# Performance work log

Hardware: AMD Instinct MI355X
Metric: run time of the kernel (lower is better)

## Reference

```python
import jax, jax.numpy as jnp
import numpy as np

D_MODEL = 1024
D_KV = 64
N_HEADS = 16
KV_HEADS = 4
G = N_HEADS // KV_HEADS
NUM_BUCKETS = 32
MAX_DISTANCE = 128


def _relative_position_bucket(relative_position, bidirectional=True,
                              num_buckets=NUM_BUCKETS, max_distance=MAX_DISTANCE):
    # Faithful port of T5Attention._relative_position_bucket
    relative_buckets = jnp.zeros_like(relative_position)
    if bidirectional:
        num_buckets //= 2
        relative_buckets = (relative_position > 0).astype(jnp.int32) * num_buckets
        relative_position = jnp.abs(relative_position)
    else:
        relative_position = -jnp.minimum(relative_position, 0)
    max_exact = num_buckets // 2
    is_small = relative_position < max_exact
    rel_if_large = max_exact + (
        jnp.log(relative_position.astype(jnp.float32) / max_exact)
        / np.log(max_distance / max_exact) * (num_buckets - max_exact)
    ).astype(jnp.int32)
    rel_if_large = jnp.minimum(rel_if_large, num_buckets - 1)
    return relative_buckets + jnp.where(is_small, relative_position, rel_if_large)


def setup_inputs() -> dict:
    key = jax.random.key(0)
    ks = jax.random.split(key, 6)
    B, S = 2, 2048
    inner = N_HEADS * D_KV
    sc = 1.0 / np.sqrt(D_MODEL)
    return {
        "hidden_states": jax.random.normal(ks[0], (B, S, D_MODEL), dtype=jnp.float32),
        "Wq": jax.random.normal(ks[1], (D_MODEL, inner), dtype=jnp.float32) * sc,
        "Wk": jax.random.normal(ks[2], (D_MODEL, inner), dtype=jnp.float32) * sc,
        "Wv": jax.random.normal(ks[3], (D_MODEL, inner), dtype=jnp.float32) * sc,
        "Wo": jax.random.normal(ks[4], (inner, D_MODEL), dtype=jnp.float32) * sc,
        "rel_bias": jax.random.normal(ks[5], (NUM_BUCKETS, N_HEADS), dtype=jnp.float32) * 0.1,
    }


def reference(hidden_states, Wq, Wk, Wv, Wo, rel_bias):
    B, S, _ = hidden_states.shape

    def split_heads(x):  # [B,S,inner] -> [B,H,S,Dk]
        return x.reshape(B, S, N_HEADS, D_KV).transpose(0, 2, 1, 3)

    q = split_heads(hidden_states @ Wq)
    k = split_heads(hidden_states @ Wk)
    v = split_heads(hidden_states @ Wv)

    # head index = g * KV_HEADS + h (einops 'b (g h) ...' with h=kv_heads)
    gq = q.reshape(B, G, KV_HEADS, S, D_KV)
    gk = k.reshape(B, G, KV_HEADS, S, D_KV).mean(axis=1)  # [B,Hkv,S,Dk]
    # einsum sums over g (as in torch.einsum 'bghnd,bhsd->bhns'); no 1/sqrt(d) in T5
    scores = jnp.einsum('bghnd,bhsd->bhns', gq, gk)  # [B,Hkv,S,S]

    # T5 relative position bias (bidirectional, encoder)
    ctx = jnp.arange(S)[:, None]
    mem = jnp.arange(S)[None, :]
    buckets = _relative_position_bucket(mem - ctx, bidirectional=True)
    bias = rel_bias[buckets]                # [S,S,H]
    bias = bias.transpose(2, 0, 1)[None]    # [1,H,S,S]
    gbias = bias.reshape(1, G, KV_HEADS, S, S).mean(axis=1)  # [1,Hkv,S,S]

    scores = scores + gbias
    attn = jax.nn.softmax(scores.astype(jnp.float32), axis=-1).astype(scores.dtype)

    # repeat grouped attn weights back to full heads: 'b h n s -> b (g h) n s'
    attn_full = jnp.tile(attn, (1, G, 1, 1))  # [B,H,S,S]
    ctx_out = jnp.einsum('bhns,bhsd->bhnd', attn_full, v)  # [B,H,S,Dk]
    ctx_out = ctx_out.transpose(0, 2, 1, 3).reshape(B, S, N_HEADS * D_KV)
    return ctx_out @ Wo  # [B,S,D_MODEL]
```

## Files before the change

### kernel.cpp

```cpp
#include <hip/hip_runtime.h>
#include <math.h>


typedef __bf16 bf16_t;
typedef bf16_t bf16x8 __attribute__((ext_vector_type(8)));
typedef bf16_t bf16x4 __attribute__((ext_vector_type(4)));
typedef float f32x4 __attribute__((ext_vector_type(4)));

#define MFMA16(a, b, c) __builtin_amdgcn_mfma_f32_16x16x32_bf16(a, b, c, 0, 0, 0)

typedef __attribute__((address_space(1))) void gvoid;
typedef __attribute__((address_space(3))) void svoid;
__device__ __forceinline__ void gld16(const void* g, void* l) {
    __builtin_amdgcn_global_load_lds((gvoid*)g, (svoid*)l, 16, 0, 0);
}

__global__ __launch_bounds__(256) void prep_all(const float* __restrict__ hs,
                                                const float* __restrict__ Wq,
                                                const float* __restrict__ Wk,
                                                const float* __restrict__ Wv,
                                                const float* __restrict__ Wo,
                                                const float* __restrict__ rel_bias,
                                                bf16_t* __restrict__ hs_hi,
                                                bf16_t* __restrict__ hs_lo,
                                                bf16_t* __restrict__ Thi,
                                                bf16_t* __restrict__ Tlo,
                                                bf16_t* __restrict__ WvT,
                                                bf16_t* __restrict__ WoT,
                                                float* __restrict__ btab) {
    __shared__ float sm[2048];
    const int r = blockIdx.x, t = threadIdx.x;
    if (r < 4096) {
        size_t idx = ((size_t)r * 256 + t) * 4;
        float4 v = *(const float4*)(hs + idx);
        bf16x4 h, l;
        h[0] = (bf16_t)v.x; l[0] = (bf16_t)(v.x - (float)h[0]);
        h[1] = (bf16_t)v.y; l[1] = (bf16_t)(v.y - (float)h[1]);
        h[2] = (bf16_t)v.z; l[2] = (bf16_t)(v.z - (float)h[2]);
        h[3] = (bf16_t)v.w; l[3] = (bf16_t)(v.w - (float)h[3]);
        *(bf16x4*)(hs_hi + idx) = h;
        *(bf16x4*)(hs_lo + idx) = l;
    } else if (r < 5120) {
        int k = r - 4096;
        float* rq = sm;
        float* rk = sm + 1024;
#pragma unroll
        for (int j = 0; j < 4; ++j) {
            rq[t + j * 256] = Wq[(size_t)k * 1024 + t + j * 256];
            rk[t + j * 256] = Wk[(size_t)k * 1024 + t + j * 256];
        }
        __syncthreads();
        int h = t >> 6, j2 = t & 63;
        float sq = 0.f, sk = 0.f;
#pragma unroll
        for (int g = 0; g < 4; ++g) {
            sq += rq[(g * 4 + h) * 64 + j2];
            sk += rk[(g * 4 + h) * 64 + j2];
        }
        sk *= 0.25f;
        bf16_t qh = (bf16_t)sq;
        Thi[(size_t)t * 1024 + k] = qh;
        Tlo[(size_t)t * 1024 + k] = (bf16_t)(sq - (float)qh);
        bf16_t kh = (bf16_t)sk;
        Thi[(size_t)(256 + t) * 1024 + k] = kh;
        Tlo[(size_t)(256 + t) * 1024 + k] = (bf16_t)(sk - (float)kh);
    } else if (r < 7168) {
        const float* src = (r < 6144) ? Wv : Wo;
        bf16_t* dst = (r < 6144) ? WvT : WoT;
        int rr = (r < 6144) ? r - 5120 : r - 6144;
        int bx = (rr & 31) * 32, by = (rr >> 5) * 32;
        int tx = t & 31, ty = t >> 5;
        float(*tile)[33] = (float(*)[33])sm;
#pragma unroll
        for (int i = 0; i < 32; i += 8)
            tile[ty + i][tx] = src[(size_t)(by + ty + i) * 1024 + bx + tx];
        __syncthreads();
#pragma unroll
        for (int i = 0; i < 32; i += 8)
            dst[(size_t)(bx + ty + i) * 1024 + by + tx] = (bf16_t)tile[tx][ty + i];
    } else {
        int idx = (r - 7168) * 256 + t;
        if (idx >= 4095) return;
        int delta = idx - 2047;
        int bucket = (delta > 0) ? 16 : 0;
        int arp = delta < 0 ? -delta : delta;
        int rb;
        if (arp < 8) {
            rb = arp;
        } else {
            float tt = (logf((float)arp * 0.125f) / 2.772588722239781f) * 8.0f;
            int ri = 8 + (int)tt;
            rb = ri < 15 ? ri : 15;
        }
        bucket += rb;
#pragma unroll
        for (int h = 0; h < 4; ++h) {
            float s = 0.25f * (rel_bias[bucket * 16 + h] + rel_bias[bucket * 16 + h + 4] +
                               rel_bias[bucket * 16 + h + 8] + rel_bias[bucket * 16 + h + 12]);
            btab[h * 4608 + idx] = s;
        }
    }
}

__global__ __launch_bounds__(256, 1) void proj_qkv(const bf16_t* __restrict__ Ah,
                                                   const bf16_t* __restrict__ Al,
                                                   const bf16_t* __restrict__ Bh,
                                                   const bf16_t* __restrict__ Bl,
                                                   const bf16_t* __restrict__ WvT,
                                                   bf16_t* __restrict__ Qhi,
                                                   bf16_t* __restrict__ Qlo,
                                                   bf16_t* __restrict__ Kbh,
                                                   bf16_t* __restrict__ Kbl,
                                                   bf16_t* __restrict__ Vb) {
    __shared__ bf16_t pool[24576];
    const int K = 1024, nk = 32;
    const int t = threadIdx.x;
    const int w = t >> 6, lane = t & 63;
    const int lr = lane & 15, q = lane >> 4;
    const int bx = blockIdx.x;
    const bool qk = bx < 8;
    const int m0 = blockIdx.y * 128;
    const int n0 = qk ? bx * 64 : (bx - 8) * 128;
    const int mw = (w & 1) * 64;
    f32x4 acc[4][4] = {};

    const int rA = t & 127, cA0 = t >> 7, cA1 = 2 + (t >> 7);
    const size_t oA0 = (size_t)(m0 + rA) * K + cA0 * 8;
    const size_t oA1 = (size_t)(m0 + rA) * K + cA1 * 8;
    const int rBq = t & 63, cBq = t >> 6;
    const size_t oBq = (size_t)(n0 + rBq) * K + cBq * 8;
    const size_t oBv0 = (size_t)(n0 + rA) * K + cA0 * 8;
    const size_t oBv1 = (size_t)(n0 + rA) * K + cA1 * 8;

    auto stage = [&](int bf, int k0) {
        gld16(Ah + oA0 + k0, &pool[bf * 4096 + t * 8]);
        gld16(Ah + oA1 + k0, &pool[bf * 4096 + (256 + t) * 8]);
        if (qk) {
            gld16(Al + oA0 + k0, &pool[8192 + bf * 4096 + t * 8]);
            gld16(Al + oA1 + k0, &pool[8192 + bf * 4096 + (256 + t) * 8]);
            gld16(Bh + oBq + k0, &pool[16384 + bf * 2048 + t * 8]);
            gld16(Bl + oBq + k0, &pool[20480 + bf * 2048 + t * 8]);
        } else {
            gld16(WvT + oBv0 + k0, &pool[8192 + bf * 4096 + t * 8]);
            gld16(WvT + oBv1 + k0, &pool[8192 + bf * 4096 + (256 + t) * 8]);
        }
    };

    stage(0, 0);
    __syncthreads();
    for (int it = 0; it < nk; ++it) {
        const int cur = it & 1;
        if (it + 1 < nk) stage(cur ^ 1, (it + 1) * 32);
        if (qk) {
            const int nw = (w >> 1) * 32;
            bf16x8 ah[4], al[4], bh[2], bl[2];
#pragma unroll
            for (int i = 0; i < 4; ++i) {
                int sa = (q * 128 + mw + i * 16 + lr) * 8;
                ah[i] = *(const bf16x8*)&pool[cur * 4096 + sa];
                al[i] = *(const bf16x8*)&pool[8192 + cur * 4096 + sa];
            }
#pragma unroll
            for (int j = 0; j < 2; ++j) {
                int sb = (q * 64 + nw + j * 16 + lr) * 8;
                bh[j] = *(const bf16x8*)&pool[16384 + cur * 2048 + sb];
                bl[j] = *(const bf16x8*)&pool[20480 + cur * 2048 + sb];
            }
#pragma unroll
            for (int i = 0; i < 4; ++i)
#pragma unroll
                for (int j = 0; j < 2; ++j) {
                    acc[i][j] = MFMA16(ah[i], bh[j], acc[i][j]);
                    acc[i][j] = MFMA16(ah[i], bl[j], acc[i][j]);
                    acc[i][j] = MFMA16(al[i], bh[j], acc[i][j]);
                }
        } else {
            const int nw = (w >> 1) * 64;
            bf16x8 af[4], bfv[4];
#pragma unroll
            for (int i = 0; i < 4; ++i)
                af[i] = *(const bf16x8*)&pool[cur * 4096 + (q * 128 + mw + i * 16 + lr) * 8];
#pragma unroll
            for (int j = 0; j < 4; ++j)
                bfv[j] =
                    *(const bf16x8*)&pool[8192 + cur * 4096 + (q * 128 + nw + j * 16 + lr) * 8];
#pragma unroll
            for (int i = 0; i < 4; ++i)
#pragma unroll
                for (int j = 0; j < 4; ++j) acc[i][j] = MFMA16(af[i], bfv[j], acc[i][j]);
        }
        __syncthreads();
    }

    const int nj = qk ? 2 : 4;
    const int nwq = qk ? (w >> 1) * 32 : (w >> 1) * 64;
#pragma unroll
    for (int i = 0; i < 4; ++i) {
        int row = m0 + mw + i * 16 + q * 4;
#pragma unroll 4
        for (int j = 0; j < nj; ++j) {
            int col = n0 + nwq + j * 16 + lr;
#pragma unroll
            for (int reg = 0; reg < 4; ++reg) {
                float x = acc[i][j][reg];
                int token = row + reg;
                if (qk) {
                    bf16_t hi = (bf16_t)x;
                    bf16_t lo = (bf16_t)(x - (float)hi);
                    if (col < 256) {
                        size_t o = (size_t)token * 256 + col;
                        Qhi[o] = hi;
                        Qlo[o] = lo;
                    } else {
                        int hc = col - 256;
                        int h = hc >> 6, d = hc & 63;
                        int b = token >> 11, s = token & 2047;
                        int it2 = s >> 6, sl = s & 63;
                        size_t o = ((size_t)((b * 4 + h) * 32 + it2)) * 4096 +
                                   (size_t)((d >> 3) * 64 + sl) * 8 + (d & 7);
                        Kbh[o] = hi;
                        Kbl[o] = lo;
                    }
                } else {
                    int vg = col;
                    int h = (vg >> 6) & 3, g = vg >> 8, d = vg & 63;
                    int b = token >> 11, s = token & 2047;
                    int it2 = s >> 6, sc = (s >> 3) & 7, si = s & 7;
                    size_t o = ((size_t)((b * 4 + h) * 32 + it2)) * 16384 +
                               (size_t)(sc * 256 + g * 64 + d) * 8 + si;
                    Vb[o] = (bf16_t)x;
                }
            }
        }
    }
}

__global__ __launch_bounds__(256, 1) void gemm_out(const bf16_t* __restrict__ A,
                                                   const bf16_t* __restrict__ BT,
                                                   float* __restrict__ C,
                                                   int M, int N, int K) {
    __shared__ bf16_t pool[12288];
    const int t = threadIdx.x;
    const int w = t >> 6, lane = t & 63;
    const int lr = lane & 15, q = lane >> 4;
    const int m0 = blockIdx.y * 128, n0 = blockIdx.x * 64;
    const int mw = (w & 1) * 64, nw = (w >> 1) * 32;
    f32x4 acc[4][2] = {};
    const int nk = K >> 5;

    const int rA = t & 127, cA0 = t >> 7, cA1 = 2 + (t >> 7);
    const bf16_t* gA0 = A + (size_t)(m0 + rA) * K + cA0 * 8;
    const bf16_t* gA1 = A + (size_t)(m0 + rA) * K + cA1 * 8;
    const bf16_t* gB = BT + (size_t)(n0 + (t & 63)) * K + (t >> 6) * 8;

    auto stage = [&](int bf, int k0) {
        gld16(gA0 + k0, &pool[bf * 4096 + t * 8]);
        gld16(gA1 + k0, &pool[bf * 4096 + (256 + t) * 8]);
        gld16(gB + k0, &pool[8192 + bf * 2048 + t * 8]);
    };

    stage(0, 0);
    __syncthreads();
    for (int it = 0; it < nk; ++it) {
        const int cur = it & 1;
        if (it + 1 < nk) stage(cur ^ 1, (it + 1) * 32);
        bf16x8 af[4], bfv[2];
#pragma unroll
        for (int i = 0; i < 4; ++i)
            af[i] = *(const bf16x8*)&pool[cur * 4096 + (q * 128 + mw + i * 16 + lr) * 8];
#pragma unroll
        for (int j = 0; j < 2; ++j)
            bfv[j] = *(const bf16x8*)&pool[8192 + cur * 2048 + (q * 64 + nw + j * 16 + lr) * 8];
#pragma unroll
        for (int i = 0; i < 4; ++i)
#pragma unroll
            for (int j = 0; j < 2; ++j) acc[i][j] = MFMA16(af[i], bfv[j], acc[i][j]);
        __syncthreads();
    }

#pragma unroll
    for (int i = 0; i < 4; ++i) {
        int row = m0 + mw + i * 16 + q * 4;
#pragma unroll
        for (int j = 0; j < 2; ++j) {
            int col = n0 + nw + j * 16 + lr;
#pragma unroll
            for (int reg = 0; reg < 4; ++reg)
                C[(size_t)(row + reg) * N + col] = acc[i][j][reg];
        }
    }
}

__global__ __launch_bounds__(512, 1) void attn_mfma(const bf16_t* __restrict__ Qhi,
                                                    const bf16_t* __restrict__ Qlo,
                                                    const bf16_t* __restrict__ Kbh,
                                                    const bf16_t* __restrict__ Kbl,
                                                    const bf16_t* __restrict__ Vb,
                                                    const float* __restrict__ btab,
                                                    bf16_t* __restrict__ part0,
                                                    bf16_t* __restrict__ part1,
                                                    float* __restrict__ Sml) {
    __shared__ bf16_t Kh[2][4096], Kl[2][4096], Vsm[2][16384], Ps[8192];
    const int t = threadIdx.x, w = t >> 6, lane = t & 63;
    const int lr = lane & 15, q = lane >> 4;
    const int blk = blockIdx.x;
    const int half = blk & 1, qt = (blk >> 1) & 15, h = (blk >> 5) & 3, b = blk >> 7;
    const int n0 = qt * 128;
    const int rowbase = n0 + w * 16;

    const size_t qrow = (size_t)(b * 2048 + rowbase + lr) * 256 + h * 64;
    bf16x8 aqh[2], aql[2];
#pragma unroll
    for (int kb = 0; kb < 2; ++kb) {
        aqh[kb] = *(const bf16x8*)(Qhi + qrow + kb * 32 + q * 8);
        aql[kb] = *(const bf16x8*)(Qlo + qrow + kb * 32 + q * 8);
    }

    const int tilebase = (b * 4 + h) * 32 + half * 16;
    const bf16_t* gK = Kbh + (size_t)tilebase * 4096;
    const bf16_t* gL = Kbl + (size_t)tilebase * 4096;
    const bf16_t* gV = Vb + (size_t)tilebase * 16384;
    const float* btabh = btab + h * 4608 + 2047;

    auto stage = [&](int bf, int it) {
        gld16(gK + (size_t)it * 4096 + t * 8, &Kh[bf][t * 8]);
        gld16(gL + (size_t)it * 4096 + t * 8, &Kl[bf][t * 8]);
        const bf16_t* v0 = gV + (size_t)it * 16384;
#pragma unroll
        for (int j = 0; j < 4; ++j)
            gld16(v0 + (j * 512 + t) * 8, &Vsm[bf][(j * 512 + t) * 8]);
    };

    float m_r[4], l_r[4];
#pragma unroll
    for (int reg = 0; reg < 4; ++reg) { m_r[reg] = -INFINITY; l_r[reg] = 0.f; }
    f32x4 O[16] = {};

    stage(0, 0);
    __syncthreads();
    for (int it = 0; it < 16; ++it) {
        const int cur = it & 1;
        if (it + 1 < 16) stage(cur ^ 1, it + 1);
        const int s0g = half * 1024 + it * 64;

        f32x4 sc[4];
#pragma unroll
        for (int ct = 0; ct < 4; ++ct) {
            f32x4 z = {0.f, 0.f, 0.f, 0.f};
#pragma unroll
            for (int kb = 0; kb < 2; ++kb) {
                int sb = ((kb * 4 + q) * 64 + ct * 16 + lr) * 8;
                bf16x8 bh = *(const bf16x8*)&Kh[cur][sb];
                bf16x8 bl = *(const bf16x8*)&Kl[cur][sb];
                z = MFMA16(aqh[kb], bh, z);
                z = MFMA16(aqh[kb], bl, z);
                z = MFMA16(aql[kb], bh, z);
            }
            sc[ct] = z;
        }
        const int dbase = (s0g + lr) - (rowbase + q * 4);
#pragma unroll
        for (int ct = 0; ct < 4; ++ct)
#pragma unroll
            for (int reg = 0; reg < 4; ++reg)
                sc[ct][reg] += btabh[dbase + ct * 16 - reg];

        float rm[4];
#pragma unroll
        for (int reg = 0; reg < 4; ++reg)
            rm[reg] = fmaxf(fmaxf(sc[0][reg], sc[1][reg]), fmaxf(sc[2][reg], sc[3][reg]));
#pragma unroll
        for (int off = 1; off < 16; off <<= 1)
#pragma unroll
            for (int reg = 0; reg < 4; ++reg)
                rm[reg] = fmaxf(rm[reg], __shfl_xor(rm[reg], off, 64));

        float alpha[4], rs[4];
#pragma unroll
        for (int reg = 0; reg < 4; ++reg) {
            float mo = m_r[reg];
            float mn = fmaxf(mo, rm[reg]);
            alpha[reg] = __expf(mo - mn);
            m_r[reg] = mn;
            rs[reg] = 0.f;
        }
#pragma unroll
        for (int ct = 0; ct < 4; ++ct) {
#pragma unroll
            for (int reg = 0; reg < 4; ++reg) {
                float p = __expf(sc[ct][reg] - m_r[reg]);
                rs[reg] += p;
                int col = ct * 16 + lr;
                Ps[((w * 128 + (col >> 3) * 16) + q * 4 + reg) * 8 + (col & 7)] = (bf16_t)p;
            }
        }
#pragma unroll
        for (int off = 1; off < 16; off <<= 1)
#pragma unroll
            for (int reg = 0; reg < 4; ++reg) rs[reg] += __shfl_xor(rs[reg], off, 64);
#pragma unroll
        for (int reg = 0; reg < 4; ++reg) l_r[reg] = l_r[reg] * alpha[reg] + rs[reg];

        bf16x8 pa[2];
#pragma unroll
        for (int kb = 0; kb < 2; ++kb)
            pa[kb] = *(const bf16x8*)&Ps[(w * 128 + (kb * 4 + q) * 16 + lr) * 8];

#pragma unroll
        for (int nt = 0; nt < 16; ++nt) {
            f32x4 o = O[nt];
#pragma unroll
            for (int reg = 0; reg < 4; ++reg) o[reg] *= alpha[reg];
#pragma unroll
            for (int kb = 0; kb < 2; ++kb) {
                bf16x8 v = *(const bf16x8*)&Vsm[cur][((kb * 4 + q) * 256 + nt * 16 + lr) * 8];
                o = MFMA16(pa[kb], v, o);
            }
            O[nt] = o;
        }
        __syncthreads();
    }

    bf16_t* P = half ? part1 : part0;
    float inv[4];
#pragma unroll
    for (int reg = 0; reg < 4; ++reg) inv[reg] = 1.f / l_r[reg];
    const size_t tokbase = (size_t)(b * 2048 + rowbase + q * 4);
#pragma unroll
    for (int nt = 0; nt < 16; ++nt) {
        int v = nt * 16 + lr;
        int vg = ((v >> 6) * 4 + h) * 64 + (v & 63);
#pragma unroll
        for (int reg = 0; reg < 4; ++reg)
            P[(tokbase + reg) * 1024 + vg] = (bf16_t)(O[nt][reg] * inv[reg]);
    }
    if (lr == 0) {
#pragma unroll
        for (int reg = 0; reg < 4; ++reg)
            Sml[half * 16384 + (tokbase + reg) * 4 + h] = m_r[reg] + logf(l_r[reg]);
    }
}

__global__ __launch_bounds__(256) void combine_halves(bf16_t* __restrict__ p0,
                                                      const bf16_t* __restrict__ p1,
                                                      const float* __restrict__ Sml) {
    size_t flat = ((size_t)blockIdx.x * 256 + threadIdx.x) * 8;
    int tok = (int)(flat >> 10), c = (int)(flat & 1023), h = (c >> 6) & 3;
    float s0 = Sml[tok * 4 + h], s1 = Sml[16384 + tok * 4 + h];
    float M = fmaxf(s0, s1);
    float e0 = __expf(s0 - M), e1 = __expf(s1 - M);
    float r = 1.f / (e0 + e1);
    float w0 = e0 * r, w1 = e1 * r;
    bf16x8 a = *(bf16x8*)(p0 + flat);
    bf16x8 bb = *(const bf16x8*)(p1 + flat);
    bf16x8 o;
#pragma unroll
    for (int i = 0; i < 8; ++i) o[i] = (bf16_t)(w0 * (float)a[i] + w1 * (float)bb[i]);
    *(bf16x8*)(p0 + flat) = o;
}

extern "C" void kernel_launch(void* const* d_in, const int* in_sizes, int n_in,
                              void* d_out, int out_size, void* d_ws, size_t ws_size,
                              hipStream_t stream) {
    const float* hs = (const float*)d_in[0];
    const float* Wq = (const float*)d_in[1];
    const float* Wk = (const float*)d_in[2];
    const float* Wv = (const float*)d_in[3];
    const float* Wo = (const float*)d_in[4];
    const float* rb = (const float*)d_in[5];
    float* out = (float*)d_out;

    const size_t MB = 1 << 20;
    const size_t KB = 1 << 10;
    char* ws = (char*)d_ws;
    bf16_t* hs_hi = (bf16_t*)(ws);
    bf16_t* hs_lo = (bf16_t*)(ws + 8 * MB);
    bf16_t* WqkThi = (bf16_t*)(ws + 16 * MB);
    bf16_t* WqkTlo = (bf16_t*)(ws + 17 * MB);
    bf16_t* WvT = (bf16_t*)(ws + 18 * MB);
    bf16_t* WoT = (bf16_t*)(ws + 20 * MB);
    float* btab = (float*)(ws + 22 * MB);
    float* Sml = (float*)(ws + 22 * MB + 128 * KB);
    bf16_t* Qhi = (bf16_t*)(ws + 22 * MB + 256 * KB);
    bf16_t* Qlo = Qhi + (size_t)4096 * 256;
    bf16_t* Kbh = Qlo + (size_t)4096 * 256;
    bf16_t* Kbl = Kbh + (size_t)4096 * 256;
    bf16_t* Vb = Kbl + (size_t)4096 * 256;
    bf16_t* part0 = hs_hi;
    bf16_t* part1 = hs_lo;

    prep_all<<<7184, 256, 0, stream>>>(hs, Wq, Wk, Wv, Wo, rb, hs_hi, hs_lo, WqkThi,
                                       WqkTlo, WvT, WoT, btab);
    proj_qkv<<<dim3(16, 32), 256, 0, stream>>>(hs_hi, hs_lo, WqkThi, WqkTlo, WvT, Qhi,
                                               Qlo, Kbh, Kbl, Vb);
    attn_mfma<<<256, 512, 0, stream>>>(Qhi, Qlo, Kbh, Kbl, Vb, btab, part0, part1, Sml);
    combine_halves<<<2048, 256, 0, stream>>>(part0, part1, Sml);
    gemm_out<<<dim3(16, 32), 256, 0, stream>>>(part0, WoT, out, 4096, 1024, 1024);
}
```

Measured before the change: 241.0 us.

## Retile attention to 64-row query blocks with 32-key tiles and 256 threads

Shrinks the attention kernel's work per block to 64 query rows and 32-key tiles with 256 threads, doubling the grid to 512 blocks, and adjusts the K/V packed layouts accordingly. The QKV projection's V path is narrowed to 64-column tiles, increasing its grid. The aim is better CU occupancy and load balance on a wide GPU, at the cost of more loop iterations, more syncs and softmax rescaling per key element.

```diff
diff --git a/kernel.cpp b/kernel.cpp
--- a/kernel.cpp
+++ b/kernel.cpp
@@ -120,29 +120,25 @@
     const int bx = blockIdx.x;
     const bool qk = bx < 8;
     const int m0 = blockIdx.y * 128;
-    const int n0 = qk ? bx * 64 : (bx - 8) * 128;
-    const int mw = (w & 1) * 64;
-    f32x4 acc[4][4] = {};
+    const int n0 = qk ? bx * 64 : (bx - 8) * 64;
+    const int mw = (w & 1) * 64, nw = (w >> 1) * 32;
+    f32x4 acc[4][2] = {};
 
     const int rA = t & 127, cA0 = t >> 7, cA1 = 2 + (t >> 7);
     const size_t oA0 = (size_t)(m0 + rA) * K + cA0 * 8;
     const size_t oA1 = (size_t)(m0 + rA) * K + cA1 * 8;
-    const int rBq = t & 63, cBq = t >> 6;
-    const size_t oBq = (size_t)(n0 + rBq) * K + cBq * 8;
-    const size_t oBv0 = (size_t)(n0 + rA) * K + cA0 * 8;
-    const size_t oBv1 = (size_t)(n0 + rA) * K + cA1 * 8;
+    const int rB = t & 63, cB = t >> 6;
+    const size_t oB = (size_t)(n0 + rB) * K + cB * 8;
+    const bf16_t* Bhi = qk ? Bh : WvT;
 
     auto stage = [&](int bf, int k0) {
         gld16(Ah + oA0 + k0, &pool[bf * 4096 + t * 8]);
         gld16(Ah + oA1 + k0, &pool[bf * 4096 + (256 + t) * 8]);
+        gld16(Bhi + oB + k0, &pool[16384 + bf * 2048 + t * 8]);
         if (qk) {
             gld16(Al + oA0 + k0, &pool[8192 + bf * 4096 + t * 8]);
             gld16(Al + oA1 + k0, &pool[8192 + bf * 4096 + (256 + t) * 8]);
-            gld16(Bh + oBq + k0, &pool[16384 + bf * 2048 + t * 8]);
-            gld16(Bl + oBq + k0, &pool[20480 + bf * 2048 + t * 8]);
-        } else {
-            gld16(WvT + oBv0 + k0, &pool[8192 + bf * 4096 + t * 8]);
-            gld16(WvT + oBv1 + k0, &pool[8192 + bf * 4096 + (256 + t) * 8]);
+            gld16(Bl + oB + k0, &pool[20480 + bf * 2048 + t * 8]);
         }
     };
 
@@ -152,7 +148,6 @@
         const int cur = it & 1;
         if (it + 1 < nk) stage(cur ^ 1, (it + 1) * 32);
         if (qk) {
-            const int nw = (w >> 1) * 32;
             bf16x8 ah[4], al[4], bh[2], bl[2];
 #pragma unroll
             for (int i = 0; i < 4; ++i) {
@@ -175,31 +170,27 @@
                     acc[i][j] = MFMA16(al[i], bh[j], acc[i][j]);
                 }
         } else {
-            const int nw = (w >> 1) * 64;
-            bf16x8 af[4], bfv[4];
+            bf16x8 af[4], bfv[2];
 #pragma unroll
             for (int i = 0; i < 4; ++i)
                 af[i] = *(const bf16x8*)&pool[cur * 4096 + (q * 128 + mw + i * 16 + lr) * 8];
 #pragma unroll
-            for (int j = 0; j < 4; ++j)
-                bfv[j] =
-                    *(const bf16x8*)&pool[8192 + cur * 4096 + (q * 128 + nw + j * 16 + lr) * 8];
+            for (int j = 0; j < 2; ++j)
+                bfv[j] = *(const bf16x8*)&pool[16384 + cur * 2048 + (q * 64 + nw + j * 16 + lr) * 8];
 #pragma unroll
             for (int i = 0; i < 4; ++i)
 #pragma unroll
-                for (int j = 0; j < 4; ++j) acc[i][j] = MFMA16(af[i], bfv[j], acc[i][j]);
+                for (int j = 0; j < 2; ++j) acc[i][j] = MFMA16(af[i], bfv[j], acc[i][j]);
         }
         __syncthreads();
     }
 
-    const int nj = qk ? 2 : 4;
-    const int nwq = qk ? (w >> 1) * 32 : (w >> 1) * 64;
 #pragma unroll
     for (int i = 0; i < 4; ++i) {
         int row = m0 + mw + i * 16 + q * 4;
-#pragma unroll 4
-        for (int j = 0; j < nj; ++j) {
-            int col = n0 + nwq + j * 16 + lr;
+#pragma unroll
+        for (int j = 0; j < 2; ++j) {
+            int col = n0 + nw + j * 16 + lr;
 #pragma unroll
             for (int reg = 0; reg < 4; ++reg) {
                 float x = acc[i][j][reg];
@@ -215,9 +206,8 @@
                         int hc = col - 256;
                         int h = hc >> 6, d = hc & 63;
                         int b = token >> 11, s = token & 2047;
-                        int it2 = s >> 6, sl = s & 63;
-                        size_t o = ((size_t)((b * 4 + h) * 32 + it2)) * 4096 +
-                                   (size_t)((d >> 3) * 64 + sl) * 8 + (d & 7);
+                        size_t o = ((size_t)((b * 4 + h) * 64 + (s >> 5))) * 2048 +
+                                   (size_t)((d >> 3) * 32 + (s & 31)) * 8 + (d & 7);
                         Kbh[o] = hi;
                         Kbl[o] = lo;
                     }
@@ -225,9 +215,8 @@
                     int vg = col;
                     int h = (vg >> 6) & 3, g = vg >> 8, d = vg & 63;
                     int b = token >> 11, s = token & 2047;
-                    int it2 = s >> 6, sc = (s >> 3) & 7, si = s & 7;
-                    size_t o = ((size_t)((b * 4 + h) * 32 + it2)) * 16384 +
-                               (size_t)(sc * 256 + g * 64 + d) * 8 + si;
+                    size_t o = ((size_t)((b * 4 + h) * 64 + (s >> 5))) * 8192 +
+                               (size_t)(((s >> 3) & 3) * 256 + g * 64 + d) * 8 + (s & 7);
                     Vb[o] = (bf16_t)x;
                 }
             }
@@ -291,7 +280,7 @@
     }
 }
 
-__global__ __launch_bounds__(512, 1) void attn_mfma(const bf16_t* __restrict__ Qhi,
+__global__ __launch_bounds__(256, 1) void attn_mfma(const bf16_t* __restrict__ Qhi,
                                                     const bf16_t* __restrict__ Qlo,
                                                     const bf16_t* __restrict__ Kbh,
                                                     const bf16_t* __restrict__ Kbl,
@@ -300,12 +289,12 @@
                                                     bf16_t* __restrict__ part0,
                                                     bf16_t* __restrict__ part1,
                                                     float* __restrict__ Sml) {
-    __shared__ bf16_t Kh[2][4096], Kl[2][4096], Vsm[2][16384], Ps[8192];
+    __shared__ bf16_t Kh[2][2048], Kl[2][2048], Vsm[2][8192], Ps[2048];
     const int t = threadIdx.x, w = t >> 6, lane = t & 63;
     const int lr = lane & 15, q = lane >> 4;
     const int blk = blockIdx.x;
-    const int half = blk & 1, qt = (blk >> 1) & 15, h = (blk >> 5) & 3, b = blk >> 7;
-    const int n0 = qt * 128;
+    const int half = blk & 1, qt = (blk >> 1) & 31, h = (blk >> 6) & 3, b = blk >> 8;
+    const int n0 = qt * 64;
     const int rowbase = n0 + w * 16;
 
     const size_t qrow = (size_t)(b * 2048 + rowbase + lr) * 256 + h * 64;
@@ -316,19 +305,19 @@
         aql[kb] = *(const bf16x8*)(Qlo + qrow + kb * 32 + q * 8);
     }
 
-    const int tilebase = (b * 4 + h) * 32 + half * 16;
-    const bf16_t* gK = Kbh + (size_t)tilebase * 4096;
-    const bf16_t* gL = Kbl + (size_t)tilebase * 4096;
-    const bf16_t* gV = Vb + (size_t)tilebase * 16384;
+    const size_t tb = (size_t)((b * 4 + h) * 64 + half * 32);
+    const bf16_t* gK = Kbh + tb * 2048;
+    const bf16_t* gL = Kbl + tb * 2048;
+    const bf16_t* gV = Vb + tb * 8192;
     const float* btabh = btab + h * 4608 + 2047;
 
     auto stage = [&](int bf, int it) {
-        gld16(gK + (size_t)it * 4096 + t * 8, &Kh[bf][t * 8]);
-        gld16(gL + (size_t)it * 4096 + t * 8, &Kl[bf][t * 8]);
-        const bf16_t* v0 = gV + (size_t)it * 16384;
+        gld16(gK + (size_t)it * 2048 + t * 8, &Kh[bf][t * 8]);
+        gld16(gL + (size_t)it * 2048 + t * 8, &Kl[bf][t * 8]);
+        const bf16_t* v0 = gV + (size_t)it * 8192;
 #pragma unroll
         for (int j = 0; j < 4; ++j)
-            gld16(v0 + (j * 512 + t) * 8, &Vsm[bf][(j * 512 + t) * 8]);
+            gld16(v0 + (j * 256 + t) * 8, &Vsm[bf][(j * 256 + t) * 8]);
     };
 
     float m_r[4], l_r[4];
@@ -338,18 +327,18 @@
 
     stage(0, 0);
     __syncthreads();
-    for (int it = 0; it < 16; ++it) {
+    for (int it = 0; it < 32; ++it) {
         const int cur = it & 1;
-        if (it + 1 < 16) stage(cur ^ 1, it + 1);
-        const int s0g = half * 1024 + it * 64;
-
-        f32x4 sc[4];
-#pragma unroll
-        for (int ct = 0; ct < 4; ++ct) {
+        if (it + 1 < 32) stage(cur ^ 1, it + 1);
+        const int s0g = half * 1024 + it * 32;
+
+        f32x4 sc[2];
+#pragma unroll
+        for (int ct = 0; ct < 2; ++ct) {
             f32x4 z = {0.f, 0.f, 0.f, 0.f};
 #pragma unroll
             for (int kb = 0; kb < 2; ++kb) {
-                int sb = ((kb * 4 + q) * 64 + ct * 16 + lr) * 8;
+                int sb = ((kb * 4 + q) * 32 + ct * 16 + lr) * 8;
                 bf16x8 bh = *(const bf16x8*)&Kh[cur][sb];
                 bf16x8 bl = *(const bf16x8*)&Kl[cur][sb];
                 z = MFMA16(aqh[kb], bh, z);
@@ -360,15 +349,14 @@
         }
         const int dbase = (s0g + lr) - (rowbase + q * 4);
 #pragma unroll
-        for (int ct = 0; ct < 4; ++ct)
+        for (int ct = 0; ct < 2; ++ct)
 #pragma unroll
             for (int reg = 0; reg < 4; ++reg)
                 sc[ct][reg] += btabh[dbase + ct * 16 - reg];
 
         float rm[4];
 #pragma unroll
-        for (int reg = 0; reg < 4; ++reg)
-            rm[reg] = fmaxf(fmaxf(sc[0][reg], sc[1][reg]), fmaxf(sc[2][reg], sc[3][reg]));
+        for (int reg = 0; reg < 4; ++reg) rm[reg] = fmaxf(sc[0][reg], sc[1][reg]);
 #pragma unroll
         for (int off = 1; off < 16; off <<= 1)
 #pragma unroll
@@ -385,13 +373,13 @@
             rs[reg] = 0.f;
         }
 #pragma unroll
-        for (int ct = 0; ct < 4; ++ct) {
+        for (int ct = 0; ct < 2; ++ct) {
 #pragma unroll
             for (int reg = 0; reg < 4; ++reg) {
                 float p = __expf(sc[ct][reg] - m_r[reg]);
                 rs[reg] += p;
                 int col = ct * 16 + lr;
-                Ps[((w * 128 + (col >> 3) * 16) + q * 4 + reg) * 8 + (col & 7)] = (bf16_t)p;
+                Ps[((w * 64 + (col >> 3) * 16) + q * 4 + reg) * 8 + (col & 7)] = (bf16_t)p;
             }
         }
 #pragma unroll
@@ -401,21 +389,15 @@
 #pragma unroll
         for (int reg = 0; reg < 4; ++reg) l_r[reg] = l_r[reg] * alpha[reg] + rs[reg];
 
-        bf16x8 pa[2];
-#pragma unroll
-        for (int kb = 0; kb < 2; ++kb)
-            pa[kb] = *(const bf16x8*)&Ps[(w * 128 + (kb * 4 + q) * 16 + lr) * 8];
+        bf16x8 pa = *(const bf16x8*)&Ps[(w * 64 + q * 16 + lr) * 8];
 
 #pragma unroll
         for (int nt = 0; nt < 16; ++nt) {
             f32x4 o = O[nt];
 #pragma unroll
             for (int reg = 0; reg < 4; ++reg) o[reg] *= alpha[reg];
-#pragma unroll
-            for (int kb = 0; kb < 2; ++kb) {
-                bf16x8 v = *(const bf16x8*)&Vsm[cur][((kb * 4 + q) * 256 + nt * 16 + lr) * 8];
-                o = MFMA16(pa[kb], v, o);
-            }
+            bf16x8 v = *(const bf16x8*)&Vsm[cur][(q * 256 + nt * 16 + lr) * 8];
+            o = MFMA16(pa, v, o);
             O[nt] = o;
         }
         __syncthreads();
@@ -491,9 +473,9 @@
 
     prep_all<<<7184, 256, 0, stream>>>(hs, Wq, Wk, Wv, Wo, rb, hs_hi, hs_lo, WqkThi,
                                        WqkTlo, WvT, WoT, btab);
-    proj_qkv<<<dim3(16, 32), 256, 0, stream>>>(hs_hi, hs_lo, WqkThi, WqkTlo, WvT, Qhi,
+    proj_qkv<<<dim3(24, 32), 256, 0, stream>>>(hs_hi, hs_lo, WqkThi, WqkTlo, WvT, Qhi,
                                                Qlo, Kbh, Kbl, Vb);
-    attn_mfma<<<256, 512, 0, stream>>>(Qhi, Qlo, Kbh, Kbl, Vb, btab, part0, part1, Sml);
+    attn_mfma<<<512, 256, 0, stream>>>(Qhi, Qlo, Kbh, Kbl, Vb, btab, part0, part1, Sml);
     combine_halves<<<2048, 256, 0, stream>>>(part0, part1, Sml);
     gemm_out<<<dim3(16, 32), 256, 0, stream>>>(part0, WoT, out, 4096, 1024, 1024);
 }
```

After: 268.4 us. 11.4% more time.
